# Performance work log

Hardware: AMD Instinct MI355X
Metric: run time of the kernel (lower is better)

The kernel has to match this reference:

```python
import jax, jax.numpy as jnp
import numpy as np
import math

B, T, C, H, L, V = 8, 511, 1024, 16, 8, 128  # T = block_size - 1
D = C // H
FF = 4 * C


def setup_inputs() -> dict:
    key = jax.random.key(0)
    ks = jax.random.split(key, 12)
    std = 0.02
    n = lambda k, s: (jax.random.normal(k, s, dtype=jnp.float32) * std)
    idx = jax.random.randint(ks[0], (B, T), 0, V)
    idx = jnp.where(idx == 2, 3, idx)  # avoid pad token so logits[idx!=2] keeps all rows
    return {
        "idx": idx,
        "tok_emb": n(ks[1], (V, C)),
        "pos_emb": n(ks[2], (T, C)),
        "ln1_w": jnp.ones((L, C)), "ln1_b": jnp.zeros((L, C)),
        "Wq": n(ks[3], (L, C, C)), "bq": jnp.zeros((L, C)),
        "Wk": n(ks[4], (L, C, C)), "bk": jnp.zeros((L, C)),
        "Wv": n(ks[5], (L, C, C)), "bv": jnp.zeros((L, C)),
        "Wp": n(ks[6], (L, C, C)), "bp": jnp.zeros((L, C)),
        "ln2_w": jnp.ones((L, C)), "ln2_b": jnp.zeros((L, C)),
        "W1": n(ks[7], (L, C, FF)), "b1": jnp.zeros((L, FF)),
        "W2": n(ks[8], (L, FF, C)), "b2": jnp.zeros((L, C)),
        "lnf_w": jnp.ones((C,)), "lnf_b": jnp.zeros((C,)),
        "head_w": n(ks[9], (V, C)),
    }


def _ln(x, w, b):
    m = x.mean(-1, keepdims=True)
    v = ((x - m) ** 2).mean(-1, keepdims=True)
    return (x - m) * jax.lax.rsqrt(v + 1e-5) * w + b


def reference(idx, tok_emb, pos_emb, ln1_w, ln1_b, Wq, bq, Wk, bk, Wv, bv, Wp, bp,
              ln2_w, ln2_b, W1, b1, W2, b2, lnf_w, lnf_b, head_w):
    x = tok_emb[idx] + pos_emb[None, :, :]                      # [B,T,C]
    mask = jnp.tril(jnp.ones((T, T), dtype=bool))
    scale = 1.0 / math.sqrt(D)

    def block(x, p):
        h = _ln(x, p["ln1_w"], p["ln1_b"])
        q = (h @ p["Wq"] + p["bq"]).reshape(B, T, H, D).transpose(0, 2, 1, 3)
        k = (h @ p["Wk"] + p["bk"]).reshape(B, T, H, D).transpose(0, 2, 1, 3)
        v = (h @ p["Wv"] + p["bv"]).reshape(B, T, H, D).transpose(0, 2, 1, 3)
        att = jnp.einsum('bhqd,bhkd->bhqk', q, k) * scale       # [B,H,T,T]
        att = jnp.where(mask, att, -jnp.inf)
        att = jax.nn.softmax(att, axis=-1)
        y = jnp.einsum('bhqk,bhkd->bhqd', att, v)
        y = y.transpose(0, 2, 1, 3).reshape(B, T, C)
        x = x + y @ p["Wp"] + p["bp"]
        h = _ln(x, p["ln2_w"], p["ln2_b"])
        h = jax.nn.gelu(h @ p["W1"] + p["b1"], approximate=False)
        x = x + h @ p["W2"] + p["b2"]
        return x, None

    stacked = dict(ln1_w=ln1_w, ln1_b=ln1_b, Wq=Wq, bq=bq, Wk=Wk, bk=bk, Wv=Wv, bv=bv,
                   Wp=Wp, bp=bp, ln2_w=ln2_w, ln2_b=ln2_b, W1=W1, b1=b1, W2=W2, b2=b2)
    x, _ = jax.lax.scan(block, x, stacked)
    x = _ln(x, lnf_w, lnf_b)
    logits = x @ head_w.T                                       # [B,T,V]
    # logits[idx != 2] with no 2-tokens present == all rows flattened
    return logits.reshape(B * T, V)
```

## Files before the change

### kernel.cpp

```cpp
#include <hip/hip_runtime.h>
#include <hip/hip_bf16.h>

typedef unsigned short u16;
typedef unsigned int   u32;
typedef __attribute__((ext_vector_type(8))) __bf16 bf16x8;
typedef __attribute__((ext_vector_type(4))) float  f32x4;

static constexpr int NB  = 8;
static constexpr int TT  = 511;
static constexpr int CC  = 1024;
static constexpr int HH  = 16;
static constexpr int LL  = 8;
static constexpr int VV  = 128;
static constexpr int FF_ = 4096;
static constexpr int MV  = NB * TT;
static constexpr int MP  = 4096;
static constexpr int TP  = 512;

#define DEVI static __device__ __forceinline__

DEVI u16 f2bf(float f) {
  u32 u = __builtin_bit_cast(u32, f);
  u = (u + 0x7fffu + ((u >> 16) & 1u)) >> 16;
  return (u16)u;
}

DEVI void gload16(const void* g, void* lds) {
  auto gp = (const __attribute__((address_space(1))) u32*)(uintptr_t)g;
  auto lp = (__attribute__((address_space(3))) u32*)(uintptr_t)lds;
  __builtin_amdgcn_global_load_lds(gp, lp, 16, 0, 0);
}

__global__ __launch_bounds__(256) void k_transpose(const float* __restrict__ in,
                                                   u16* __restrict__ out, int K, int N,
                                                   size_t is, size_t os) {
  in  += (size_t)blockIdx.z * is;
  out += (size_t)blockIdx.z * os;
  __shared__ u16 tile[64][66];
  int nb = blockIdx.x * 64, kb = blockIdx.y * 64;
  int t = threadIdx.x;
  int r = t >> 4, c4 = (t & 15) * 4;
#pragma unroll
  for (int i = 0; i < 4; ++i) {
    int k = r + i * 16;
    float4 v = *(const float4*)(in + (size_t)(kb + k) * N + nb + c4);
    tile[k][c4 + 0] = f2bf(v.x); tile[k][c4 + 1] = f2bf(v.y);
    tile[k][c4 + 2] = f2bf(v.z); tile[k][c4 + 3] = f2bf(v.w);
  }
  __syncthreads();
#pragma unroll
  for (int i = 0; i < 4; ++i) {
    int n = r + i * 16;
    ushort4 o;
    o.x = tile[c4 + 0][n]; o.y = tile[c4 + 1][n];
    o.z = tile[c4 + 2][n]; o.w = tile[c4 + 3][n];
    *(ushort4*)(out + (size_t)(nb + n) * K + kb + c4) = o;
  }
}

__global__ __launch_bounds__(256) void k_cast_bf16(const float* __restrict__ in,
                                                   u16* __restrict__ out, int n) {
  int i = blockIdx.x * 256 + threadIdx.x;
  if (i < n) out[i] = f2bf(in[i]);
}

__global__ __launch_bounds__(256) void k_pack_qkv_bias(const float* __restrict__ bq,
                                                       const float* __restrict__ bk,
                                                       const float* __restrict__ bv,
                                                       float* __restrict__ out) {
  int i = blockIdx.x * 256 + threadIdx.x;
  int l = i / (3 * CC), c = i % (3 * CC);
  float v = (c < CC) ? bq[l * CC + c] : (c < 2 * CC) ? bk[l * CC + c - CC] : bv[l * CC + c - 2 * CC];
  out[i] = v;
}

__global__ __launch_bounds__(256) void k_embed(const int* __restrict__ idx,
                                               const float* __restrict__ tok,
                                               const float* __restrict__ pos,
                                               float* __restrict__ x) {
  int row = blockIdx.x;
  int c4 = threadIdx.x * 4;
  if (row >= MV) {
    *(float4*)(x + (size_t)row * CC + c4) = make_float4(0.f, 0.f, 0.f, 0.f);
    return;
  }
  int t = row % TT;
  int tid = idx[row];
  float4 a = *(const float4*)(tok + (size_t)tid * CC + c4);
  float4 p = *(const float4*)(pos + (size_t)t * CC + c4);
  a.x += p.x; a.y += p.y; a.z += p.z; a.w += p.w;
  *(float4*)(x + (size_t)row * CC + c4) = a;
}

__global__ __launch_bounds__(256) void k_ln(const float* __restrict__ x,
                                            const float* __restrict__ w,
                                            const float* __restrict__ b,
                                            u16* __restrict__ out) {
  int wid = threadIdx.x >> 6, l = threadIdx.x & 63;
  int row = blockIdx.x * 4 + wid;
  const float* xr = x + (size_t)row * CC;
  float4 v[4];
  float s = 0.f, sq = 0.f;
#pragma unroll
  for (int i = 0; i < 4; ++i) {
    v[i] = *(const float4*)(xr + (i * 64 + l) * 4);
    s  += v[i].x + v[i].y + v[i].z + v[i].w;
    sq += v[i].x * v[i].x + v[i].y * v[i].y + v[i].z * v[i].z + v[i].w * v[i].w;
  }
#pragma unroll
  for (int o = 32; o; o >>= 1) { s += __shfl_xor(s, o); sq += __shfl_xor(sq, o); }
  float mean = s * (1.f / CC);
  float var  = sq * (1.f / CC) - mean * mean;
  float rs = rsqrtf(var + 1e-5f);
#pragma unroll
  for (int i = 0; i < 4; ++i) {
    int c = (i * 64 + l) * 4;
    float4 wv = *(const float4*)(w + c);
    float4 bv = *(const float4*)(b + c);
    ushort4 o4;
    o4.x = f2bf((v[i].x - mean) * rs * wv.x + bv.x);
    o4.y = f2bf((v[i].y - mean) * rs * wv.y + bv.y);
    o4.z = f2bf((v[i].z - mean) * rs * wv.z + bv.z);
    o4.w = f2bf((v[i].w - mean) * rs * wv.w + bv.w);
    *(ushort4*)(out + (size_t)row * CC + c) = o4;
  }
}

template <int BN, int EPI, int KSPLIT>
__global__ __launch_bounds__(512, 2) void k_gemm2(const u16* __restrict__ A,
                                                  const u16* __restrict__ Wt,
                                                  const float* __restrict__ bias,
                                                  float* __restrict__ outf,
                                                  u16* __restrict__ outb,
                                                  int N, int K, int gridN, int Mv) {
  constexpr int WN  = BN / 64;
  constexpr int GLB = BN / 64;
  constexpr int GL  = 4 + GLB;
  constexpr int ATILE = 256 * 64;
  __shared__ u16 lds[2][ATILE + BN * 64];

  int t = threadIdx.x, l = t & 63, wid = t >> 6;
  int wr = wid >> 2, wc = wid & 3;
  int lr = l & 15, lk16 = (l >> 4) * 16;

  int nwg = gridDim.x, wg = blockIdx.x;
  int q = nwg >> 3, r = nwg & 7;
  int xcd = wg & 7, loc = wg >> 3;
  int swz = (xcd < r ? xcd * (q + 1) : r * (q + 1) + (xcd - r) * q) + loc;
  int mblk = swz / (gridN * KSPLIT);
  int rest = swz - mblk * (gridN * KSPLIT);
  int nblk = rest / KSPLIT;
  int kz   = rest - nblk * KSPLIT;
  int mb = mblk * 256, nb = nblk * BN;
  int Ksub = K / KSPLIT;
  int NT = Ksub >> 6;
  const u16* Ab = A  + (size_t)mb * K + (size_t)kz * Ksub;
  const u16* Bb = Wt + (size_t)nb * K + (size_t)kz * Ksub;

  int srow8 = t >> 3;
  int skb   = (t & 7) * 16;

  auto stage = [&](int kt, int b) {
    const u16* As = Ab + kt * 64;
#pragma unroll
    for (int j = 0; j < 4; ++j) {
      int row = j * 64 + srow8;
      int kb  = skb ^ ((row & 7) << 4);
      gload16(As + (size_t)row * K + (kb >> 1), &lds[b][j * 4096 + wid * 512]);
    }
    const u16* Bs = Bb + kt * 64;
#pragma unroll
    for (int j = 0; j < GLB; ++j) {
      int row = j * 64 + srow8;
      int kb  = skb ^ ((row & 7) << 4);
      gload16(Bs + (size_t)row * K + (kb >> 1), &lds[b][ATILE + j * 4096 + wid * 512]);
    }
  };

  f32x4 acc[8][WN] = {};

  auto tile = [&](int b) {
    const char* LA = (const char*)&lds[b][0];
    const char* LB = (const char*)&lds[b][ATILE];
    bf16x8 bf[2][WN];
#pragma unroll
    for (int ks = 0; ks < 2; ++ks)
#pragma unroll
      for (int n = 0; n < WN; ++n) {
        int rr = wc * (WN * 16) + n * 16 + lr;
        int kb = (ks * 64 + lk16) ^ ((rr & 7) << 4);
        bf[ks][n] = *(const bf16x8*)(LB + rr * 128 + kb);
      }
#pragma unroll
    for (int half = 0; half < 2; ++half) {
      bf16x8 af[2][4];
#pragma unroll
      for (int ks = 0; ks < 2; ++ks)
#pragma unroll
        for (int m = 0; m < 4; ++m) {
          int rr = wr * 128 + (half * 64) + m * 16 + lr;
          int kb = (ks * 64 + lk16) ^ ((rr & 7) << 4);
          af[ks][m] = *(const bf16x8*)(LA + rr * 128 + kb);
        }
      __builtin_amdgcn_s_setprio(1);
#pragma unroll
      for (int ks = 0; ks < 2; ++ks)
#pragma unroll
        for (int m = 0; m < 4; ++m)
#pragma unroll
          for (int n = 0; n < WN; ++n)
            acc[half * 4 + m][n] = __builtin_amdgcn_mfma_f32_16x16x32_bf16(
                af[ks][m], bf[ks][n], acc[half * 4 + m][n], 0, 0, 0);
      __builtin_amdgcn_s_setprio(0);
    }
  };

  stage(0, 0);
  stage(1, 1);
  asm volatile("s_waitcnt vmcnt(%0)" :: "n"(GL) : "memory");
  __builtin_amdgcn_s_barrier();
  __builtin_amdgcn_sched_barrier(0);

  for (int kt = 0; kt < NT; kt += 2) {
#pragma unroll
    for (int sub = 0; sub < 2; ++sub) {
      tile(sub);
      asm volatile("s_waitcnt lgkmcnt(0)" ::: "memory");
      __builtin_amdgcn_s_barrier();
      __builtin_amdgcn_sched_barrier(0);
      if (kt + 2 + sub < NT) {
        stage(kt + 2 + sub, sub);
        asm volatile("s_waitcnt vmcnt(%0)" :: "n"(GL) : "memory");
      } else {
        asm volatile("s_waitcnt vmcnt(0)" ::: "memory");
      }
      __builtin_amdgcn_s_barrier();
      __builtin_amdgcn_sched_barrier(0);
    }
  }

  int r0 = (l >> 4) * 4;
#pragma unroll
  for (int m = 0; m < 8; ++m) {
    int gr = mb + wr * 128 + m * 16 + r0;
#pragma unroll
    for (int n = 0; n < WN; ++n) {
      int gc = nb + wc * (WN * 16) + n * 16 + lr;
      float bv;
      if constexpr (EPI == 4) bv = (kz == 0 && bias) ? bias[gc] : 0.f;
      else bv = bias[gc];
#pragma unroll
      for (int rr = 0; rr < 4; ++rr) {
        int grr = gr + rr;
        float v = acc[m][n][rr] + bv;
        size_t o = (size_t)grr * N + gc;
        if constexpr (EPI == 1) {
          outb[o] = f2bf(v);
        } else if constexpr (EPI == 2) {
          float g = 0.5f * v * (1.0f + erff(v * 0.70710678f));
          outb[o] = f2bf(g);
        } else {
          if (grr < Mv) atomicAdd(outf + o, v);
        }
      }
    }
  }
}

__global__ __launch_bounds__(256) void k_vtrans(const u16* __restrict__ qkv,
                                                u16* __restrict__ vt) {
  __shared__ u16 tile[64][66];
  int bh = blockIdx.y;
  int b = bh >> 4, h = bh & 15;
  int t0 = blockIdx.x * 64;
  int t = threadIdx.x;
  int r = t >> 4, c4 = (t & 15) * 4;
#pragma unroll
  for (int i = 0; i < 4; ++i) {
    int tt = r + i * 16;
    int trow = t0 + tt;
    int srow = b * TT + (trow < TT ? trow : TT - 1);
    ushort4 v = *(const ushort4*)(qkv + (size_t)srow * 3072 + 2048 + h * 64 + c4);
    tile[tt][c4 + 0] = v.x; tile[tt][c4 + 1] = v.y;
    tile[tt][c4 + 2] = v.z; tile[tt][c4 + 3] = v.w;
  }
  __syncthreads();
#pragma unroll
  for (int i = 0; i < 4; ++i) {
    int d = r + i * 16;
    ushort4 o;
    o.x = (t0 + c4 + 0 < TT) ? tile[c4 + 0][d] : (u16)0;
    o.y = (t0 + c4 + 1 < TT) ? tile[c4 + 1][d] : (u16)0;
    o.z = (t0 + c4 + 2 < TT) ? tile[c4 + 2][d] : (u16)0;
    o.w = (t0 + c4 + 3 < TT) ? tile[c4 + 3][d] : (u16)0;
    *(ushort4*)(vt + ((size_t)bh * 64 + d) * TP + t0 + c4) = o;
  }
}

__global__ __launch_bounds__(512, 2) void k_attn2(const u16* __restrict__ qkv,
                                                  const u16* __restrict__ vt,
                                                  u16* __restrict__ y) {
  __shared__ u16 Kb[2][64 * 64];
  __shared__ u16 Vb[2][64 * 64];
  __shared__ u16 Pb[8][16 * 64];
  int t = threadIdx.x, l = t & 63, w = t >> 6;

  int nwg = gridDim.x, wg = blockIdx.x;
  int swz = (wg & 7) * (nwg >> 3) + (wg >> 3);
  int bh = swz >> 2, qt = swz & 3;
  int b = bh >> 4, h = bh & 15;
  int q0 = qt * 128;
  int lr = l & 15, lg = l >> 4, lk8 = lg * 8;

  const float ISC = 0.125f;

  bf16x8 Qa[2];
  {
    int qs = q0 + w * 16 + lr;
    const u16* qp = qkv + (size_t)(b * TT + (qs < TT ? qs : TT - 1)) * 3072 + h * 64;
    Qa[0] = *(const bf16x8*)(qp + lk8);
    Qa[1] = *(const bf16x8*)(qp + 32 + lk8);
  }

  int NT = (q0 + 128) >> 6;

  int srow = w * 8 + (l >> 3);
  int sb16 = (l & 7) * 16;
  int bcol = sb16 ^ ((srow & 7) << 4);
  const u16* Ksrc = qkv + 1024 + h * 64;
  const char* Vsrc = (const char*)(vt + ((size_t)bh * 64 + srow) * TP);

  auto stage = [&](int kt, int buf) {
    int kv0 = kt * 64;
    int kvr = kv0 + srow;
    int krow = b * TT + (kvr < TT ? kvr : TT - 1);
    gload16((const char*)(Ksrc + (size_t)krow * 3072) + bcol, (char*)&Kb[buf][0] + t * 16);
    gload16(Vsrc + kv0 * 2 + bcol, (char*)&Vb[buf][0] + t * 16);
  };

  f32x4 O[4] = {};
  float m_[4], s_[4];
#pragma unroll
  for (int r = 0; r < 4; ++r) { m_[r] = -1e30f; s_[r] = 0.f; }

  stage(0, 0);
  for (int kt = 0; kt < NT; ++kt) {
    int buf = kt & 1;
    if (kt + 1 < NT) {
      stage(kt + 1, buf ^ 1);
      asm volatile("s_waitcnt vmcnt(2)" ::: "memory");
    } else {
      asm volatile("s_waitcnt vmcnt(0)" ::: "memory");
    }
    __builtin_amdgcn_s_barrier();

    int kv0 = kt * 64;
    f32x4 S[4];
    const char* LK = (const char*)&Kb[buf][0];
#pragma unroll
    for (int j = 0; j < 4; ++j) {
      f32x4 a = {};
#pragma unroll
      for (int ks = 0; ks < 2; ++ks) {
        int row = j * 16 + lr;
        int kb = ((ks * 32 + lk8) * 2) ^ ((row & 7) << 4);
        bf16x8 kf = *(const bf16x8*)(LK + row * 128 + kb);
        a = __builtin_amdgcn_mfma_f32_16x16x32_bf16(Qa[ks], kf, a, 0, 0, 0);
      }
      S[j] = a;
    }
    int qbase = q0 + w * 16 + lg * 4;
#pragma unroll
    for (int j = 0; j < 4; ++j) {
      int kv = kv0 + j * 16 + lr;
#pragma unroll
      for (int r = 0; r < 4; ++r) {
        bool valid = (kv <= qbase + r) && (kv < TT);
        S[j][r] = valid ? S[j][r] : -1e30f;
      }
    }
    float mx[4];
#pragma unroll
    for (int r = 0; r < 4; ++r)
      mx[r] = fmaxf(fmaxf(S[0][r], S[1][r]), fmaxf(S[2][r], S[3][r]));
#pragma unroll
    for (int r = 0; r < 4; ++r) {
      mx[r] = fmaxf(mx[r], __shfl_xor(mx[r], 1));
      mx[r] = fmaxf(mx[r], __shfl_xor(mx[r], 2));
      mx[r] = fmaxf(mx[r], __shfl_xor(mx[r], 4));
      mx[r] = fmaxf(mx[r], __shfl_xor(mx[r], 8));
    }
    float sc[4];
#pragma unroll
    for (int r = 0; r < 4; ++r) {
      float mn = fmaxf(m_[r], mx[r]);
      sc[r] = __expf((m_[r] - mn) * ISC);
      m_[r] = mn;
      s_[r] *= sc[r];
    }
#pragma unroll
    for (int j = 0; j < 4; ++j)
#pragma unroll
      for (int r = 0; r < 4; ++r) O[j][r] *= sc[r];
    float rs[4] = {0.f, 0.f, 0.f, 0.f};
    char* LP = (char*)&Pb[w][0];
#pragma unroll
    for (int j = 0; j < 4; ++j) {
#pragma unroll
      for (int r = 0; r < 4; ++r) {
        float p = __expf((S[j][r] - m_[r]) * ISC);
        rs[r] += p;
        int row = lg * 4 + r;
        int addr = (row * 128 + (j * 16 + lr) * 2) ^ ((row & 7) << 4);
        *(u16*)(LP + addr) = f2bf(p);
      }
    }
#pragma unroll
    for (int r = 0; r < 4; ++r) {
      rs[r] += __shfl_xor(rs[r], 1);
      rs[r] += __shfl_xor(rs[r], 2);
      rs[r] += __shfl_xor(rs[r], 4);
      rs[r] += __shfl_xor(rs[r], 8);
      s_[r] += rs[r];
    }
    bf16x8 Pa[2];
#pragma unroll
    for (int ks = 0; ks < 2; ++ks) {
      int addr = (lr * 128 + (ks * 32 + lk8) * 2) ^ ((lr & 7) << 4);
      Pa[ks] = *(const bf16x8*)(LP + addr);
    }
    const char* LV = (const char*)&Vb[buf][0];
#pragma unroll
    for (int j = 0; j < 4; ++j) {
#pragma unroll
      for (int ks = 0; ks < 2; ++ks) {
        int row = j * 16 + lr;
        int kb = ((ks * 32 + lk8) * 2) ^ ((row & 7) << 4);
        bf16x8 vf = *(const bf16x8*)(LV + row * 128 + kb);
        O[j] = __builtin_amdgcn_mfma_f32_16x16x32_bf16(Pa[ks], vf, O[j], 0, 0, 0);
      }
    }
    asm volatile("s_waitcnt lgkmcnt(0)" ::: "memory");
    __builtin_amdgcn_s_barrier();
  }

  int qs0 = q0 + w * 16 + lg * 4;
#pragma unroll
  for (int r = 0; r < 4; ++r) {
    float inv = 1.0f / s_[r];
    int qs = qs0 + r;
    if (qs < TT) {
      u16* yp = y + (size_t)(b * TT + qs) * CC + h * 64;
#pragma unroll
      for (int j = 0; j < 4; ++j)
        yp[j * 16 + lr] = f2bf(O[j][r] * inv);
    }
  }
}

extern "C" void kernel_launch(void* const* d_in, const int* in_sizes, int n_in,
                              void* d_out, int out_size, void* d_ws, size_t ws_size,
                              hipStream_t stream) {
  (void)in_sizes; (void)n_in; (void)ws_size;
  const int*   idx  = (const int*)  d_in[0];
  const float* tok  = (const float*)d_in[1];
  const float* pos  = (const float*)d_in[2];
  const float* ln1w = (const float*)d_in[3];
  const float* ln1b = (const float*)d_in[4];
  const float* Wq   = (const float*)d_in[5];
  const float* bq   = (const float*)d_in[6];
  const float* Wk   = (const float*)d_in[7];
  const float* bk   = (const float*)d_in[8];
  const float* Wv   = (const float*)d_in[9];
  const float* bv   = (const float*)d_in[10];
  const float* Wp   = (const float*)d_in[11];
  const float* bp   = (const float*)d_in[12];
  const float* ln2w = (const float*)d_in[13];
  const float* ln2b = (const float*)d_in[14];
  const float* W1   = (const float*)d_in[15];
  const float* b1   = (const float*)d_in[16];
  const float* W2   = (const float*)d_in[17];
  const float* b2   = (const float*)d_in[18];
  const float* lnfw = (const float*)d_in[19];
  const float* lnfb = (const float*)d_in[20];
  const float* headw= (const float*)d_in[21];
  float* out = (float*)d_out;

  char* p = (char*)d_ws;
  auto alloc = [&](size_t bytes) { char* r = p; p += (bytes + 255) & ~(size_t)255; return r; };
  u16*   wqkv_t = (u16*)  alloc((size_t)LL * 3 * CC * CC * 2);
  u16*   wp_t   = (u16*)  alloc((size_t)LL * CC * CC * 2);
  u16*   w1_t   = (u16*)  alloc((size_t)LL * FF_ * CC * 2);
  u16*   w2_t   = (u16*)  alloc((size_t)LL * CC * FF_ * 2);
  u16*   headb  = (u16*)  alloc((size_t)VV * CC * 2);
  float* bqkv   = (float*)alloc((size_t)LL * 3 * CC * 4);
  float* x      = (float*)alloc((size_t)MP * CC * 4);
  u16*   hbuf   = (u16*)  alloc((size_t)MP * CC * 2);
  u16*   qkv    = (u16*)  alloc((size_t)MP * 3 * CC * 2);
  u16*   vt     = (u16*)  alloc((size_t)NB * HH * 64 * TP * 2);
  u16*   ybuf   = (u16*)  alloc((size_t)MP * CC * 2);
  u16*   ffb    = (u16*)  alloc((size_t)MP * FF_ * 2);

  hipMemsetAsync(out, 0, (size_t)out_size * 4, stream);

  k_transpose<<<dim3(16, 16, LL), 256, 0, stream>>>(Wq, wqkv_t,                      CC, CC, (size_t)CC * CC, (size_t)3 * CC * CC);
  k_transpose<<<dim3(16, 16, LL), 256, 0, stream>>>(Wk, wqkv_t + (size_t)CC * CC,    CC, CC, (size_t)CC * CC, (size_t)3 * CC * CC);
  k_transpose<<<dim3(16, 16, LL), 256, 0, stream>>>(Wv, wqkv_t + (size_t)2 * CC * CC,CC, CC, (size_t)CC * CC, (size_t)3 * CC * CC);
  k_transpose<<<dim3(16, 16, LL), 256, 0, stream>>>(Wp, wp_t,                        CC, CC, (size_t)CC * CC, (size_t)CC * CC);
  k_transpose<<<dim3(64, 16, LL), 256, 0, stream>>>(W1, w1_t,                        CC, FF_, (size_t)CC * FF_, (size_t)FF_ * CC);
  k_transpose<<<dim3(16, 64, LL), 256, 0, stream>>>(W2, w2_t,                        FF_, CC, (size_t)FF_ * CC, (size_t)CC * FF_);
  k_cast_bf16<<<(VV * CC + 255) / 256, 256, 0, stream>>>(headw, headb, VV * CC);
  k_pack_qkv_bias<<<(LL * 3 * CC) / 256, 256, 0, stream>>>(bq, bk, bv, bqkv);

  k_embed<<<MP, 256, 0, stream>>>(idx, tok, pos, x);

  for (int l = 0; l < LL; ++l) {
    k_ln<<<MP / 4, 256, 0, stream>>>(x, ln1w + (size_t)l * CC, ln1b + (size_t)l * CC, hbuf);
    k_gemm2<256, 1, 1><<<12 * 16, 512, 0, stream>>>(hbuf, wqkv_t + (size_t)l * 3 * CC * CC,
                                                    bqkv + (size_t)l * 3 * CC, nullptr, qkv, 3 * CC, CC, 12, MP);
    k_vtrans<<<dim3(8, NB * HH), 256, 0, stream>>>(qkv, vt);
    k_attn2<<<NB * HH * 4, 512, 0, stream>>>(qkv, vt, ybuf);
    k_gemm2<128, 4, 2><<<8 * 16 * 2, 512, 0, stream>>>(ybuf, wp_t + (size_t)l * CC * CC,
                                                       bp + (size_t)l * CC, x, nullptr, CC, CC, 8, MP);
    k_ln<<<MP / 4, 256, 0, stream>>>(x, ln2w + (size_t)l * CC, ln2b + (size_t)l * CC, hbuf);
    k_gemm2<256, 2, 1><<<16 * 16, 512, 0, stream>>>(hbuf, w1_t + (size_t)l * FF_ * CC,
                                                    b1 + (size_t)l * FF_, nullptr, ffb, FF_, CC, 16, MP);
    k_gemm2<128, 4, 2><<<8 * 16 * 2, 512, 0, stream>>>(ffb, w2_t + (size_t)l * CC * FF_,
                                                       b2 + (size_t)l * CC, x, nullptr, CC, FF_, 8, MP);
  }

  k_ln<<<MP / 4, 256, 0, stream>>>(x, lnfw, lnfb, hbuf);
  k_gemm2<128, 4, 4><<<16 * 1 * 4, 512, 0, stream>>>(hbuf, headb, nullptr, out, nullptr, VV, CC, 1, MV);
}
```

Baseline: 2.021 ms.

## Replace split-K atomic GEMMs with 128x128 tile GEMM writing residual directly

```diff
diff --git a/kernel.cpp b/kernel.cpp
--- a/kernel.cpp
+++ b/kernel.cpp
@@ -246,9 +246,7 @@
 #pragma unroll
     for (int n = 0; n < WN; ++n) {
       int gc = nb + wc * (WN * 16) + n * 16 + lr;
-      float bv;
-      if constexpr (EPI == 4) bv = (kz == 0 && bias) ? bias[gc] : 0.f;
-      else bv = bias[gc];
+      float bv = bias[gc];
 #pragma unroll
       for (int rr = 0; rr < 4; ++rr) {
         int grr = gr + rr;
@@ -256,11 +254,137 @@
         size_t o = (size_t)grr * N + gc;
         if constexpr (EPI == 1) {
           outb[o] = f2bf(v);
-        } else if constexpr (EPI == 2) {
+        } else {
           float g = 0.5f * v * (1.0f + erff(v * 0.70710678f));
           outb[o] = f2bf(g);
+        }
+      }
+    }
+  }
+}
+
+template <int EPI>
+__global__ __launch_bounds__(256, 2) void k_gemm3(const u16* __restrict__ A,
+                                                  const u16* __restrict__ Wt,
+                                                  const float* __restrict__ bias,
+                                                  float* __restrict__ outf,
+                                                  const float* __restrict__ resid,
+                                                  int N, int K, int gridN, int Mv) {
+  constexpr int BTILE = 16384;
+  __shared__ u16 lds[2][128 * 64 * 2];
+
+  int t = threadIdx.x, l = t & 63, wid = t >> 6;
+  int wr = wid >> 1, wc = wid & 1;
+  int lr = l & 15, lk16 = (l >> 4) * 16;
+
+  int nwg = gridDim.x, wg = blockIdx.x;
+  int q = nwg >> 3, r = nwg & 7;
+  int xcd = wg & 7, loc = wg >> 3;
+  int swz = (xcd < r ? xcd * (q + 1) : r * (q + 1) + (xcd - r) * q) + loc;
+  int mblk = swz / gridN;
+  int nblk = swz - mblk * gridN;
+  int mb = mblk * 128, nb = nblk * 128;
+  int NT = K >> 6;
+  const u16* Ab = A  + (size_t)mb * K;
+  const u16* Bb = Wt + (size_t)nb * K;
+
+  int srow = t >> 3;
+  int skb  = (t & 7) * 16;
+
+  auto stage = [&](int kt, int b) {
+    const u16* As = Ab + kt * 64;
+    char* LD = (char*)&lds[b][0];
+#pragma unroll
+    for (int j = 0; j < 4; ++j) {
+      int row = j * 32 + srow;
+      int kb  = skb ^ ((row & 7) << 4);
+      gload16(As + (size_t)row * K + (kb >> 1), LD + j * 4096 + t * 16);
+    }
+    const u16* Bs = Bb + kt * 64;
+#pragma unroll
+    for (int j = 0; j < 4; ++j) {
+      int row = j * 32 + srow;
+      int kb  = skb ^ ((row & 7) << 4);
+      gload16(Bs + (size_t)row * K + (kb >> 1), LD + BTILE + j * 4096 + t * 16);
+    }
+  };
+
+  f32x4 acc[4][4] = {};
+
+  auto tile = [&](int b) {
+    const char* LA = (const char*)&lds[b][0];
+    const char* LB = LA + BTILE;
+    bf16x8 bfr[2][4], afr[2][4];
+#pragma unroll
+    for (int ks = 0; ks < 2; ++ks)
+#pragma unroll
+      for (int n = 0; n < 4; ++n) {
+        int rr = wc * 64 + n * 16 + lr;
+        int kb = (ks * 64 + lk16) ^ ((rr & 7) << 4);
+        bfr[ks][n] = *(const bf16x8*)(LB + rr * 128 + kb);
+      }
+#pragma unroll
+    for (int ks = 0; ks < 2; ++ks)
+#pragma unroll
+      for (int m = 0; m < 4; ++m) {
+        int rr = wr * 64 + m * 16 + lr;
+        int kb = (ks * 64 + lk16) ^ ((rr & 7) << 4);
+        afr[ks][m] = *(const bf16x8*)(LA + rr * 128 + kb);
+      }
+    __builtin_amdgcn_s_setprio(1);
+#pragma unroll
+    for (int ks = 0; ks < 2; ++ks)
+#pragma unroll
+      for (int m = 0; m < 4; ++m)
+#pragma unroll
+        for (int n = 0; n < 4; ++n)
+          acc[m][n] = __builtin_amdgcn_mfma_f32_16x16x32_bf16(
+              afr[ks][m], bfr[ks][n], acc[m][n], 0, 0, 0);
+    __builtin_amdgcn_s_setprio(0);
+  };
+
+  stage(0, 0);
+  stage(1, 1);
+  asm volatile("s_waitcnt vmcnt(8)" ::: "memory");
+  __builtin_amdgcn_s_barrier();
+  __builtin_amdgcn_sched_barrier(0);
+
+  for (int kt = 0; kt < NT; kt += 2) {
+#pragma unroll
+    for (int sub = 0; sub < 2; ++sub) {
+      tile(sub);
+      asm volatile("s_waitcnt lgkmcnt(0)" ::: "memory");
+      __builtin_amdgcn_s_barrier();
+      __builtin_amdgcn_sched_barrier(0);
+      if (kt + 2 + sub < NT) {
+        stage(kt + 2 + sub, sub);
+        asm volatile("s_waitcnt vmcnt(8)" ::: "memory");
+      } else {
+        asm volatile("s_waitcnt vmcnt(0)" ::: "memory");
+      }
+      __builtin_amdgcn_s_barrier();
+      __builtin_amdgcn_sched_barrier(0);
+    }
+  }
+
+  int r0 = (l >> 4) * 4;
+#pragma unroll
+  for (int m = 0; m < 4; ++m) {
+    int gr = mb + wr * 64 + m * 16 + r0;
+#pragma unroll
+    for (int n = 0; n < 4; ++n) {
+      int gc = nb + wc * 64 + n * 16 + lr;
+      float bv = 0.f;
+      if constexpr (EPI == 0) bv = bias[gc];
+#pragma unroll
+      for (int rr = 0; rr < 4; ++rr) {
+        int grr = gr + rr;
+        float v = acc[m][n][rr] + bv;
+        size_t o = (size_t)grr * N + gc;
+        if constexpr (EPI == 0) {
+          outf[o] = v + resid[o];
         } else {
-          if (grr < Mv) atomicAdd(outf + o, v);
+          if (grr < Mv) outf[o] = v;
         }
       }
     }
@@ -461,7 +585,7 @@
 extern "C" void kernel_launch(void* const* d_in, const int* in_sizes, int n_in,
                               void* d_out, int out_size, void* d_ws, size_t ws_size,
                               hipStream_t stream) {
-  (void)in_sizes; (void)n_in; (void)ws_size;
+  (void)in_sizes; (void)n_in; (void)out_size; (void)ws_size;
   const int*   idx  = (const int*)  d_in[0];
   const float* tok  = (const float*)d_in[1];
   const float* pos  = (const float*)d_in[2];
@@ -501,8 +625,6 @@
   u16*   ybuf   = (u16*)  alloc((size_t)MP * CC * 2);
   u16*   ffb    = (u16*)  alloc((size_t)MP * FF_ * 2);
 
-  hipMemsetAsync(out, 0, (size_t)out_size * 4, stream);
-
   k_transpose<<<dim3(16, 16, LL), 256, 0, stream>>>(Wq, wqkv_t,                      CC, CC, (size_t)CC * CC, (size_t)3 * CC * CC);
   k_transpose<<<dim3(16, 16, LL), 256, 0, stream>>>(Wk, wqkv_t + (size_t)CC * CC,    CC, CC, (size_t)CC * CC, (size_t)3 * CC * CC);
   k_transpose<<<dim3(16, 16, LL), 256, 0, stream>>>(Wv, wqkv_t + (size_t)2 * CC * CC,CC, CC, (size_t)CC * CC, (size_t)3 * CC * CC);
@@ -520,15 +642,15 @@
                                                     bqkv + (size_t)l * 3 * CC, nullptr, qkv, 3 * CC, CC, 12, MP);
     k_vtrans<<<dim3(8, NB * HH), 256, 0, stream>>>(qkv, vt);
     k_attn2<<<NB * HH * 4, 512, 0, stream>>>(qkv, vt, ybuf);
-    k_gemm2<128, 4, 2><<<8 * 16 * 2, 512, 0, stream>>>(ybuf, wp_t + (size_t)l * CC * CC,
-                                                       bp + (size_t)l * CC, x, nullptr, CC, CC, 8, MP);
+    k_gemm3<0><<<32 * 8, 256, 0, stream>>>(ybuf, wp_t + (size_t)l * CC * CC,
+                                           bp + (size_t)l * CC, x, x, CC, CC, 8, MP);
     k_ln<<<MP / 4, 256, 0, stream>>>(x, ln2w + (size_t)l * CC, ln2b + (size_t)l * CC, hbuf);
     k_gemm2<256, 2, 1><<<16 * 16, 512, 0, stream>>>(hbuf, w1_t + (size_t)l * FF_ * CC,
                                                     b1 + (size_t)l * FF_, nullptr, ffb, FF_, CC, 16, MP);
-    k_gemm2<128, 4, 2><<<8 * 16 * 2, 512, 0, stream>>>(ffb, w2_t + (size_t)l * CC * FF_,
-                                                       b2 + (size_t)l * CC, x, nullptr, CC, FF_, 8, MP);
+    k_gemm3<0><<<32 * 8, 256, 0, stream>>>(ffb, w2_t + (size_t)l * CC * FF_,
+                                           b2 + (size_t)l * CC, x, x, CC, FF_, 8, MP);
   }
 
   k_ln<<<MP / 4, 256, 0, stream>>>(x, lnfw, lnfb, hbuf);
-  k_gemm2<128, 4, 4><<<16 * 1 * 4, 512, 0, stream>>>(hbuf, headb, nullptr, out, nullptr, VV, CC, 1, MV);
-}
+  k_gemm3<3><<<32 * 1, 256, 0, stream>>>(hbuf, headb, nullptr, out, nullptr, VV, CC, 1, MV);
+}
```

Result: faster. 1.716 ms (-15.1%).
